# Kernel optimization log

Hardware: AMD Instinct MI355X
Metric: run time of the kernel (lower is better)

The kernel has to match this reference:

```python
import jax, jax.numpy as jnp
import numpy as np
import math

B, S, D, H = 2, 2048, 1024, 16
HD = D // H  # head_dims = 64


def setup_inputs() -> dict:
    key = jax.random.key(0)
    ks = jax.random.split(key, 8)
    sc = 1.0 / math.sqrt(D)
    return {
        "queries": jax.random.normal(ks[0], (B, S, D), jnp.float32),
        "keys":    jax.random.normal(ks[1], (B, S, D), jnp.float32),
        "values":  jax.random.normal(ks[2], (B, S, D), jnp.float32),
        # causal mask: 1 where attending allowed, 0 where blocked (masked_fill on ==0)
        "mask": jnp.tril(jnp.ones((S, S), jnp.int32)),
        "Wq": jax.random.normal(ks[3], (D, D), jnp.float32) * sc,
        "bq": jnp.zeros((D,), jnp.float32),
        "Wk": jax.random.normal(ks[4], (D, D), jnp.float32) * sc,
        "bk": jnp.zeros((D,), jnp.float32),
        "Wv": jax.random.normal(ks[5], (D, D), jnp.float32) * sc,
        "bv": jnp.zeros((D,), jnp.float32),
        "Wo": jax.random.normal(ks[6], (D, D), jnp.float32) * sc,
        "bo": jnp.zeros((D,), jnp.float32),
    }


def _split_heads(x):
    # (B, S, D) -> (B, H, S, HD)
    return x.reshape(B, S, H, HD).transpose(0, 2, 1, 3)


def reference(queries, keys, values, mask, Wq, bq, Wk, bk, Wv, bv, Wo, bo):
    q = queries @ Wq + bq
    k = keys @ Wk + bk
    # NOTE: faithful to source quirk — V is projected from the ALREADY-PROJECTED keys
    # (original: keys = self.W_keys(keys); values = self.W_values(keys))
    v = k @ Wv + bv
    q, k, v = _split_heads(q), _split_heads(k), _split_heads(v)
    # naive full NxN attention, as in the source
    scores = jnp.einsum("bhqd,bhkd->bhqk", q, k) / math.sqrt(HD)
    scores = jnp.where(mask == 0, jnp.float32(-1e9), scores)
    probs = jax.nn.softmax(scores, axis=-1)
    attn = jnp.einsum("bhqk,bhkd->bhqd", probs, v)
    attn = attn.transpose(0, 2, 1, 3).reshape(B, S, D)
    return attn @ Wo + bo
```

## Files before the change

### kernel.cpp

```cpp
#include <hip/hip_runtime.h>

typedef unsigned short u16;
typedef unsigned int u32;
typedef __bf16 bf16x8 __attribute__((ext_vector_type(8)));
typedef float f32x4 __attribute__((ext_vector_type(4)));
typedef float f32x16 __attribute__((ext_vector_type(16)));
typedef unsigned int u32x4v __attribute__((ext_vector_type(4)));

#define MFMA16(a, b, c) __builtin_amdgcn_mfma_f32_16x16x32_bf16(a, b, c, 0, 0, 0)
#define MFMA32(a, b, c) __builtin_amdgcn_mfma_f32_32x32x16_bf16(a, b, c, 0, 0, 0)

__device__ __forceinline__ void gload16(const void* g, void* l) {
  __builtin_amdgcn_global_load_lds((const __attribute__((address_space(1))) void*)g,
                                   (__attribute__((address_space(3))) void*)l, 16, 0, 0);
}

__device__ __forceinline__ u16 f2bf(float f) {
  u32 u = __builtin_bit_cast(u32, f);
  u += 0x7fffu + ((u >> 16) & 1u);
  return (u16)(u >> 16);
}
__device__ __forceinline__ u32 pack2(float a, float b) {
  return (u32)f2bf(a) | ((u32)f2bf(b) << 16);
}

__global__ __launch_bounds__(256) void cvt_kernel(const float* __restrict__ q,
                                                  const float* __restrict__ k,
                                                  u16* __restrict__ qb,
                                                  u16* __restrict__ kb) {
  const float* src = blockIdx.y ? k : q;
  u16* dst = blockIdx.y ? kb : qb;
  size_t i = (size_t)blockIdx.x * 256 + threadIdx.x;
  float4 v = ((const float4*)src)[i];
  ushort4 o;
  o.x = f2bf(v.x); o.y = f2bf(v.y); o.z = f2bf(v.z); o.w = f2bf(v.w);
  ((ushort4*)dst)[i] = o;
}

__global__ __launch_bounds__(256) void wtrans_kernel(const float* W0, const float* W1,
                                                     const float* W2, const float* W3,
                                                     u16* T0, u16* T1, u16* T2, u16* T3) {
  int z = blockIdx.z;
  const float* W = z == 0 ? W0 : z == 1 ? W1 : z == 2 ? W2 : W3;
  u16* T = z == 0 ? T0 : z == 1 ? T1 : z == 2 ? T2 : T3;
  __shared__ float tile[64][65];
  int tr = blockIdx.y * 64, tc = blockIdx.x * 64;
  int tid = threadIdx.x;
  int c4 = (tid & 15) * 4, r0 = tid >> 4;
#pragma unroll
  for (int i = 0; i < 4; i++) {
    int r = r0 + i * 16;
    float4 v = *(const float4*)(W + (size_t)(tr + r) * 1024 + tc + c4);
    tile[r][c4 + 0] = v.x; tile[r][c4 + 1] = v.y;
    tile[r][c4 + 2] = v.z; tile[r][c4 + 3] = v.w;
  }
  __syncthreads();
#pragma unroll
  for (int i = 0; i < 2; i++) {
    int c = tid + i * 256;
    int n = c >> 3, kg = c & 7;
    uint4 o;
    o.x = pack2(tile[kg * 8 + 0][n], tile[kg * 8 + 1][n]);
    o.y = pack2(tile[kg * 8 + 2][n], tile[kg * 8 + 3][n]);
    o.z = pack2(tile[kg * 8 + 4][n], tile[kg * 8 + 5][n]);
    o.w = pack2(tile[kg * 8 + 6][n], tile[kg * 8 + 7][n]);
    *(uint4*)(T + (size_t)(tc + n) * 1024 + tr + kg * 8) = o;
  }
}

template <int MODE>
__global__ __launch_bounds__(256) void gemm_kernel(
    const u16* A0, const u16* B0, const float* bias0, void* C0, float scale0,
    const u16* A1, const u16* B1, const float* bias1, void* C1, float scale1,
    int M, int N, int K) {
  const u16* A = A0; const u16* Bt = B0; const float* bias = bias0; void* Cout = C0;
  float scale = scale0;
  if (blockIdx.z) { A = A1; Bt = B1; bias = bias1; Cout = C1; scale = scale1; }

  __shared__ __attribute__((aligned(16))) char sAB[49152];
  const int tid = threadIdx.x, lane = tid & 63, w = tid >> 6;
  const int l15 = lane & 15, quad = lane >> 4;
  const int wm = (w >> 1) * 64, wn = (w & 1) * 32;
  const int m0 = blockIdx.y * 128, n0 = blockIdx.x * 64;

  const int lrow = lane >> 3, lcg = (lane & 7) ^ lrow;
  const u16* aP[4]; const u16* bP[2];
#pragma unroll
  for (int i = 0; i < 4; i++)
    aP[i] = A + (size_t)(m0 + w * 32 + i * 8 + lrow) * K + lcg * 8;
#pragma unroll
  for (int i = 0; i < 2; i++)
    bP[i] = Bt + (size_t)(n0 + w * 16 + i * 8 + lrow) * K + lcg * 8;

  int aoff[4], boff[2];
#pragma unroll
  for (int t = 0; t < 4; t++) {
    int ra = wm + t * 16 + l15;
    aoff[t] = ra * 128 + ((quad ^ (ra & 7)) * 16);
  }
#pragma unroll
  for (int t = 0; t < 2; t++) {
    int rb = wn + t * 16 + l15;
    boff[t] = 16384 + rb * 128 + ((quad ^ (rb & 7)) * 16);
  }

#pragma unroll
  for (int i = 0; i < 4; i++) { gload16(aP[i], sAB + w * 4096 + i * 1024); aP[i] += 64; }
#pragma unroll
  for (int i = 0; i < 2; i++) { gload16(bP[i], sAB + 16384 + w * 2048 + i * 1024); bP[i] += 64; }

  f32x4 acc[4][2] = {};
  int cur = 0;
  for (int k = 0; k < K; k += 64) {
    __syncthreads();
    if (k + 64 < K) {
      char* dst = sAB + (cur ^ 1) * 24576;
#pragma unroll
      for (int i = 0; i < 4; i++) { gload16(aP[i], dst + w * 4096 + i * 1024); aP[i] += 64; }
#pragma unroll
      for (int i = 0; i < 2; i++) { gload16(bP[i], dst + 16384 + w * 2048 + i * 1024); bP[i] += 64; }
    }
    const char* buf = sAB + cur * 24576;
#pragma unroll
    for (int kt = 0; kt < 2; kt++) {
      bf16x8 af[4], bfr[2];
#pragma unroll
      for (int t = 0; t < 4; t++) af[t] = *(const bf16x8*)(buf + (aoff[t] ^ (kt * 64)));
#pragma unroll
      for (int t = 0; t < 2; t++) bfr[t] = *(const bf16x8*)(buf + (boff[t] ^ (kt * 64)));
#pragma unroll
      for (int mt = 0; mt < 4; mt++)
#pragma unroll
        for (int nt = 0; nt < 2; nt++)
          acc[mt][nt] = MFMA16(af[mt], bfr[nt], acc[mt][nt]);
    }
    cur ^= 1;
  }

#pragma unroll
  for (int nt = 0; nt < 2; nt++) {
    int col = n0 + wn + nt * 16 + l15;
    float bv = bias[col];
#pragma unroll
    for (int mt = 0; mt < 4; mt++) {
      int row = m0 + wm + mt * 16 + quad * 4;
      if (MODE == 0) {
        u16* C = (u16*)Cout;
#pragma unroll
        for (int r = 0; r < 4; r++)
          C[(size_t)(row + r) * N + col] = f2bf((acc[mt][nt][r] + bv) * scale);
      } else if (MODE == 1) {
        u16* C = (u16*)Cout;
        int hh = col >> 6, hd = col & 63;
        int bb = row >> 11, s = row & 2047;
        ushort4 o;
        o.x = f2bf((acc[mt][nt][0] + bv) * scale);
        o.y = f2bf((acc[mt][nt][1] + bv) * scale);
        o.z = f2bf((acc[mt][nt][2] + bv) * scale);
        o.w = f2bf((acc[mt][nt][3] + bv) * scale);
        *(ushort4*)(C + ((size_t)((bb * 16 + hh) * 64 + hd) * 2048 + s)) = o;
      } else {
        float* C = (float*)Cout;
#pragma unroll
        for (int r = 0; r < 4; r++)
          C[(size_t)(row + r) * N + col] = (acc[mt][nt][r] + bv) * scale;
      }
    }
  }
}

__global__ __launch_bounds__(256, 2) void attn_kernel(const u16* __restrict__ qw,
                                                      const u16* __restrict__ kw,
                                                      const u16* __restrict__ vw,
                                                      u16* __restrict__ aout) {
  __shared__ __attribute__((aligned(16))) char sKV[4][16384];
  const int bh = blockIdx.x, p = blockIdx.y;
  const int b = bh >> 4, h = bh & 15;
  const int tid = threadIdx.x, lane = tid & 63, w = tid >> 6;
  const int g = w & 1, qh = w >> 1;
  const int c = lane & 31, hi = lane >> 5;
  const int qcol = qh * 32 + c;
  const int lrow = lane >> 3, lcg = (lane & 7) ^ lrow;
  const u16* kb0 = kw + (size_t)(b * 2048) * 1024 + h * 64;
  const u16* vb0 = vw + (size_t)bh * 64 * 2048;

  int kvoff[2][4];
#pragma unroll
  for (int m = 0; m < 2; m++)
#pragma unroll
    for (int kt = 0; kt < 4; kt++) {
      int row = m * 32 + c;
      kvoff[m][kt] = row * 128 + (((kt * 2 + hi) ^ (row & 7)) * 16);
    }

  auto stage = [&](int j, int slot) {
    char* dst = sKV[slot];
#pragma unroll
    for (int i = 0; i < 2; i++) {
      int rr = w * 16 + i * 8 + lrow;
      gload16(kb0 + (size_t)(j * 64 + rr) * 1024 + lcg * 8, dst + w * 2048 + i * 1024);
      gload16(vb0 + (size_t)rr * 2048 + j * 64 + lcg * 8, dst + 8192 + w * 2048 + i * 1024);
    }
  };

  for (int phase = 0; phase < 2; ++phase) {
    const int t = phase ? (31 - p) : p;
    __syncthreads();

    bf16x8 qf[4];
    {
      const u16* qbase =
          qw + (size_t)(b * 2048 + t * 64 + qcol) * 1024 + h * 64 + hi * 8;
#pragma unroll
      for (int kt = 0; kt < 4; kt++) qf[kt] = *(const bf16x8*)(qbase + kt * 16);
    }
    stage(0, 0);
    if (t >= 1) stage(1, 1);

    f32x16 o0 = {}, o1 = {};
    float lsum = 0.f;
    const int R = (t + 2) >> 1;
    for (int r = 0; r < R; ++r) {
      __syncthreads();
      if (2 * r + 2 <= t) stage(2 * r + 2, (2 * r + 2) & 3);
      if (2 * r + 3 <= t) stage(2 * r + 3, (2 * r + 3) & 3);
      const int jg = 2 * r + g;
      if (jg <= t) {
        const char* buf = sKV[jg & 3];
        f32x16 S0 = {}, S1 = {};
        __builtin_amdgcn_s_setprio(1);
#pragma unroll
        for (int kt = 0; kt < 4; kt++) {
          bf16x8 k0 = *(const bf16x8*)(buf + kvoff[0][kt]);
          bf16x8 k1 = *(const bf16x8*)(buf + kvoff[1][kt]);
          S0 = MFMA32(k0, qf[kt], S0);
          S1 = MFMA32(k1, qf[kt], S1);
        }
        __builtin_amdgcn_s_setprio(0);
        const bool diag = (jg == t);
        u32 pw0[8], pw1[8];
        auto epack = [&](const f32x16& S, int mbase, u32* pw) {
          float e[16];
#pragma unroll
          for (int rg = 0; rg < 16; rg++) {
            float ev = __builtin_amdgcn_exp2f(S[rg]);
            if (diag) {
              int row = mbase + (rg & 3) + 8 * (rg >> 2) + 4 * hi;
              if (row > qcol) ev = 0.f;
            }
            e[rg] = ev;
          }
          float s = 0.f;
#pragma unroll
          for (int rg = 0; rg < 16; rg += 4)
            s += (e[rg] + e[rg + 1]) + (e[rg + 2] + e[rg + 3]);
          lsum += s;
#pragma unroll
          for (int i = 0; i < 8; i++) pw[i] = pack2(e[2 * i], e[2 * i + 1]);
        };
        epack(S0, 0, pw0);
        epack(S1, 32, pw1);
        __builtin_amdgcn_s_setprio(1);
#pragma unroll
        for (int kt2 = 0; kt2 < 4; kt2++) {
          const u32* pws = (kt2 < 2) ? pw0 : pw1;
          const int bb = (kt2 & 1) * 4;
          auto s0 = __builtin_amdgcn_permlane32_swap(pws[bb + 0], pws[bb + 2], false, false);
          auto s1 = __builtin_amdgcn_permlane32_swap(pws[bb + 1], pws[bb + 3], false, false);
          u32x4v pq = {s0[0], s1[0], s0[1], s1[1]};
          bf16x8 pf = __builtin_bit_cast(bf16x8, pq);
          bf16x8 v0 = *(const bf16x8*)(buf + 8192 + kvoff[0][kt2]);
          bf16x8 v1 = *(const bf16x8*)(buf + 8192 + kvoff[1][kt2]);
          o0 = MFMA32(v0, pf, o0);
          o1 = MFMA32(v1, pf, o1);
        }
        __builtin_amdgcn_s_setprio(0);
      }
    }

    __syncthreads();
    if (g == 1) {
      float* red = (float*)(sKV[0] + qh * 8448);
      float* redl = (float*)(sKV[0] + qh * 8448 + 8192);
#pragma unroll
      for (int rg = 0; rg < 16; rg++) {
        red[lane * 32 + rg] = o0[rg];
        red[lane * 32 + 16 + rg] = o1[rg];
      }
      redl[lane] = lsum;
    }
    __syncthreads();
    if (g == 0) {
      const float* red = (const float*)(sKV[0] + qh * 8448);
      const float* redl = (const float*)(sKV[0] + qh * 8448 + 8192);
#pragma unroll
      for (int rg = 0; rg < 16; rg++) {
        o0[rg] += red[lane * 32 + rg];
        o1[rg] += red[lane * 32 + 16 + rg];
      }
      lsum += redl[lane];
      lsum += __shfl_xor(lsum, 32, 64);
      float inv = 1.0f / lsum;
      int token = b * 2048 + t * 64 + qcol;
      u16* outp = aout + (size_t)token * 1024 + h * 64;
#pragma unroll
      for (int i = 0; i < 4; i++) {
        ushort4 ov;
        ov.x = f2bf(o0[4 * i + 0] * inv);
        ov.y = f2bf(o0[4 * i + 1] * inv);
        ov.z = f2bf(o0[4 * i + 2] * inv);
        ov.w = f2bf(o0[4 * i + 3] * inv);
        *(ushort4*)(outp + i * 8 + hi * 4) = ov;
        ov.x = f2bf(o1[4 * i + 0] * inv);
        ov.y = f2bf(o1[4 * i + 1] * inv);
        ov.z = f2bf(o1[4 * i + 2] * inv);
        ov.w = f2bf(o1[4 * i + 3] * inv);
        *(ushort4*)(outp + 32 + i * 8 + hi * 4) = ov;
      }
    }
  }
}

extern "C" void kernel_launch(void* const* d_in, const int* in_sizes, int n_in,
                              void* d_out, int out_size, void* d_ws, size_t ws_size,
                              hipStream_t stream) {
  const float* queries = (const float*)d_in[0];
  const float* keys    = (const float*)d_in[1];
  const float* Wq = (const float*)d_in[4];
  const float* bq = (const float*)d_in[5];
  const float* Wk = (const float*)d_in[6];
  const float* bk = (const float*)d_in[7];
  const float* Wv = (const float*)d_in[8];
  const float* bv = (const float*)d_in[9];
  const float* Wo = (const float*)d_in[10];
  const float* bo = (const float*)d_in[11];

  char* ws = (char*)d_ws;
  u16* qb  = (u16*)(ws);
  u16* kb  = (u16*)(ws + (8u << 20));
  u16* qP  = (u16*)(ws + (16u << 20));
  u16* kP  = (u16*)(ws);
  u16* vP  = (u16*)(ws + (8u << 20));
  u16* WqT = (u16*)(ws + (24u << 20));
  u16* WkT = (u16*)(ws + (26u << 20));
  u16* WvT = (u16*)(ws + (28u << 20));
  u16* WoT = (u16*)(ws + (30u << 20));

  const float kscale = 1.4426950408889634f / 8.0f;

  cvt_kernel<<<dim3(4096, 2), 256, 0, stream>>>(queries, keys, qb, kb);
  wtrans_kernel<<<dim3(16, 16, 4), 256, 0, stream>>>(Wq, Wk, Wv, Wo, WqT, WkT, WvT, WoT);
  gemm_kernel<0><<<dim3(16, 32, 2), 256, 0, stream>>>(
      qb, WqT, bq, qP, kscale, kb, WkT, bk, kP, 1.0f, 4096, 1024, 1024);
  gemm_kernel<1><<<dim3(16, 32, 1), 256, 0, stream>>>(
      kP, WvT, bv, vP, 1.0f, kP, WvT, bv, vP, 1.0f, 4096, 1024, 1024);
  attn_kernel<<<dim3(32, 16), 256, 0, stream>>>(qP, kP, vP, qP);
  gemm_kernel<2><<<dim3(16, 32, 1), 256, 0, stream>>>(
      qP, WoT, bo, d_out, 1.0f, qP, WoT, bo, d_out, 1.0f, 4096, 1024, 1024);
}
```

Measured before the change: 216.1 us.

## Widen GEMM tile to 128x128 and use triple-buffered LDS pipeline

The projection GEMMs now use 128x128 block tiles, with each wave computing 64x64, so every LDS fragment feeds more MFMAs. The shared-memory loop changes from double to triple buffering, staging two tiles ahead and waiting with vmcnt instead of a full sync. This is meant to improve data reuse and hide global-load latency. In exchange, LDS use grows to 96KB, which can limit occupancy, and the grid shrinks to 256 or 512 blocks, which may underfill the 256 CUs.

```diff
diff --git a/kernel.cpp b/kernel.cpp
--- a/kernel.cpp
+++ b/kernel.cpp
@@ -77,68 +77,87 @@
   float scale = scale0;
   if (blockIdx.z) { A = A1; Bt = B1; bias = bias1; Cout = C1; scale = scale1; }
 
-  __shared__ __attribute__((aligned(16))) char sAB[49152];
+  __shared__ __attribute__((aligned(16))) char sAB[98304];
   const int tid = threadIdx.x, lane = tid & 63, w = tid >> 6;
   const int l15 = lane & 15, quad = lane >> 4;
-  const int wm = (w >> 1) * 64, wn = (w & 1) * 32;
-  const int m0 = blockIdx.y * 128, n0 = blockIdx.x * 64;
+  const int wm = (w >> 1) * 64, wn = (w & 1) * 64;
+  const int m0 = blockIdx.y * 128, n0 = blockIdx.x * 128;
 
   const int lrow = lane >> 3, lcg = (lane & 7) ^ lrow;
-  const u16* aP[4]; const u16* bP[2];
+  const u16* aP[4]; const u16* bP[4];
 #pragma unroll
   for (int i = 0; i < 4; i++)
     aP[i] = A + (size_t)(m0 + w * 32 + i * 8 + lrow) * K + lcg * 8;
 #pragma unroll
-  for (int i = 0; i < 2; i++)
-    bP[i] = Bt + (size_t)(n0 + w * 16 + i * 8 + lrow) * K + lcg * 8;
-
-  int aoff[4], boff[2];
+  for (int i = 0; i < 4; i++)
+    bP[i] = Bt + (size_t)(n0 + w * 32 + i * 8 + lrow) * K + lcg * 8;
+
+  int aoff[4], boff[4];
 #pragma unroll
   for (int t = 0; t < 4; t++) {
     int ra = wm + t * 16 + l15;
     aoff[t] = ra * 128 + ((quad ^ (ra & 7)) * 16);
   }
 #pragma unroll
-  for (int t = 0; t < 2; t++) {
+  for (int t = 0; t < 4; t++) {
     int rb = wn + t * 16 + l15;
     boff[t] = 16384 + rb * 128 + ((quad ^ (rb & 7)) * 16);
   }
 
-#pragma unroll
-  for (int i = 0; i < 4; i++) { gload16(aP[i], sAB + w * 4096 + i * 1024); aP[i] += 64; }
-#pragma unroll
-  for (int i = 0; i < 2; i++) { gload16(bP[i], sAB + 16384 + w * 2048 + i * 1024); bP[i] += 64; }
-
-  f32x4 acc[4][2] = {};
-  int cur = 0;
-  for (int k = 0; k < K; k += 64) {
-    __syncthreads();
-    if (k + 64 < K) {
-      char* dst = sAB + (cur ^ 1) * 24576;
-#pragma unroll
-      for (int i = 0; i < 4; i++) { gload16(aP[i], dst + w * 4096 + i * 1024); aP[i] += 64; }
-#pragma unroll
-      for (int i = 0; i < 2; i++) { gload16(bP[i], dst + 16384 + w * 2048 + i * 1024); bP[i] += 64; }
-    }
-    const char* buf = sAB + cur * 24576;
+  auto stage = [&](char* dst) {
+#pragma unroll
+    for (int i = 0; i < 4; i++) { gload16(aP[i], dst + w * 4096 + i * 1024); aP[i] += 64; }
+#pragma unroll
+    for (int i = 0; i < 4; i++) { gload16(bP[i], dst + 16384 + w * 4096 + i * 1024); bP[i] += 64; }
+  };
+
+  const int NIT = K >> 6;
+  stage(sAB);
+  if (NIT > 1) stage(sAB + 32768);
+
+  f32x4 acc[4][4] = {};
+  for (int i = 0; i < NIT - 1; ++i) {
+    asm volatile("s_waitcnt vmcnt(8)" ::: "memory");
+    __builtin_amdgcn_s_barrier();
+    asm volatile("" ::: "memory");
+    if (i + 2 < NIT) stage(sAB + ((i + 2) % 3) * 32768);
+    const char* buf = sAB + (i % 3) * 32768;
 #pragma unroll
     for (int kt = 0; kt < 2; kt++) {
-      bf16x8 af[4], bfr[2];
+      bf16x8 af[4], bfr[4];
 #pragma unroll
       for (int t = 0; t < 4; t++) af[t] = *(const bf16x8*)(buf + (aoff[t] ^ (kt * 64)));
 #pragma unroll
-      for (int t = 0; t < 2; t++) bfr[t] = *(const bf16x8*)(buf + (boff[t] ^ (kt * 64)));
+      for (int t = 0; t < 4; t++) bfr[t] = *(const bf16x8*)(buf + (boff[t] ^ (kt * 64)));
 #pragma unroll
       for (int mt = 0; mt < 4; mt++)
 #pragma unroll
-        for (int nt = 0; nt < 2; nt++)
+        for (int nt = 0; nt < 4; nt++)
           acc[mt][nt] = MFMA16(af[mt], bfr[nt], acc[mt][nt]);
     }
-    cur ^= 1;
-  }
-
-#pragma unroll
-  for (int nt = 0; nt < 2; nt++) {
+  }
+  {
+    asm volatile("s_waitcnt vmcnt(0)" ::: "memory");
+    __builtin_amdgcn_s_barrier();
+    asm volatile("" ::: "memory");
+    const char* buf = sAB + ((NIT - 1) % 3) * 32768;
+#pragma unroll
+    for (int kt = 0; kt < 2; kt++) {
+      bf16x8 af[4], bfr[4];
+#pragma unroll
+      for (int t = 0; t < 4; t++) af[t] = *(const bf16x8*)(buf + (aoff[t] ^ (kt * 64)));
+#pragma unroll
+      for (int t = 0; t < 4; t++) bfr[t] = *(const bf16x8*)(buf + (boff[t] ^ (kt * 64)));
+#pragma unroll
+      for (int mt = 0; mt < 4; mt++)
+#pragma unroll
+        for (int nt = 0; nt < 4; nt++)
+          acc[mt][nt] = MFMA16(af[mt], bfr[nt], acc[mt][nt]);
+    }
+  }
+
+#pragma unroll
+  for (int nt = 0; nt < 4; nt++) {
     int col = n0 + wn + nt * 16 + l15;
     float bv = bias[col];
 #pragma unroll
@@ -350,11 +369,11 @@
 
   cvt_kernel<<<dim3(4096, 2), 256, 0, stream>>>(queries, keys, qb, kb);
   wtrans_kernel<<<dim3(16, 16, 4), 256, 0, stream>>>(Wq, Wk, Wv, Wo, WqT, WkT, WvT, WoT);
-  gemm_kernel<0><<<dim3(16, 32, 2), 256, 0, stream>>>(
+  gemm_kernel<0><<<dim3(8, 32, 2), 256, 0, stream>>>(
       qb, WqT, bq, qP, kscale, kb, WkT, bk, kP, 1.0f, 4096, 1024, 1024);
-  gemm_kernel<1><<<dim3(16, 32, 1), 256, 0, stream>>>(
+  gemm_kernel<1><<<dim3(8, 32, 1), 256, 0, stream>>>(
       kP, WvT, bv, vP, 1.0f, kP, WvT, bv, vP, 1.0f, 4096, 1024, 1024);
   attn_kernel<<<dim3(32, 16), 256, 0, stream>>>(qP, kP, vP, qP);
-  gemm_kernel<2><<<dim3(16, 32, 1), 256, 0, stream>>>(
+  gemm_kernel<2><<<dim3(8, 32, 1), 256, 0, stream>>>(
       qP, WoT, bo, d_out, 1.0f, qP, WoT, bo, d_out, 1.0f, 4096, 1024, 1024);
 }
```

After: 221.0 us. +2.2%, slower.
